# Kernel tuning notes

Hardware: AMD Instinct MI355X
Metric: run time of the kernel (lower is better)

## Reference

```python
import jax, jax.numpy as jnp
import numpy as np

EPS = 1e-5

def _bn(h, gamma, beta):
    # BatchNorm1d in training mode: batch stats over dim 0, biased variance
    mu = h.mean(axis=0)
    var = ((h - mu) ** 2).mean(axis=0)
    return gamma * (h - mu) * jax.lax.rsqrt(var + EPS) + beta

def _gnn_layer(x, w, src, dst, Wv, bv, We, be, g_n, b_n, g_e, b_e):
    n_nodes = x.shape[0]
    # 4 node linears: Wv [4,d,d], bv [4,d]
    xl = jnp.einsum('nd,kfd->knf', x, Wv) + bv[:, None, :]  # [4, N, d]
    x1, x2, x3, x4 = xl[0], xl[1], xl[2], xl[3]
    # sigmoid-gated messages, mean-aggregated to source nodes
    msg = jax.nn.sigmoid(w) * x2[dst]                         # [E, d]
    agg = jax.ops.segment_sum(msg, src, num_segments=n_nodes)
    cnt = jax.ops.segment_sum(jnp.ones((src.shape[0], 1), x.dtype), src,
                              num_segments=n_nodes)
    agg = agg / jnp.maximum(cnt, 1.0)
    x_new = x + jax.nn.silu(_bn(x1 + agg, g_n, b_n))
    w_new = w + jax.nn.silu(_bn(w @ We.T + be + x3[src] + x4[dst], g_e, b_e))
    return x_new, w_new

def setup_inputs() -> dict:
    key = jax.random.key(0)
    N, E, D, L = 50000, 800000, 64, 3
    ks = jax.random.split(key, 10)
    x = jax.random.normal(ks[0], (N, D), dtype=jnp.float32)
    edge_index = jax.random.randint(ks[1], (2, E), 0, N, dtype=jnp.int64)
    edge_attr = jax.random.normal(ks[2], (E, D), dtype=jnp.float32)
    Wv = jax.random.normal(ks[3], (L, 4, D, D), dtype=jnp.float32) * 0.05
    bv = jax.random.normal(ks[4], (L, 4, D), dtype=jnp.float32) * 0.05
    We = jax.random.normal(ks[5], (L, D, D), dtype=jnp.float32) * 0.05
    be = jax.random.normal(ks[6], (L, D), dtype=jnp.float32) * 0.05
    g_node = jnp.ones((L, D), dtype=jnp.float32)
    b_node = jnp.zeros((L, D), dtype=jnp.float32)
    g_edge = jnp.ones((L, D), dtype=jnp.float32)
    b_edge = jnp.zeros((L, D), dtype=jnp.float32)
    return {"x": x, "edge_index": edge_index, "edge_attr": edge_attr,
            "Wv": Wv, "bv": bv, "We": We, "be": be,
            "g_node": g_node, "b_node": b_node,
            "g_edge": g_edge, "b_edge": b_edge}

def reference(x, edge_index, edge_attr, Wv, bv, We, be,
              g_node, b_node, g_edge, b_edge):
    src, dst = edge_index[0], edge_index[1]
    h = jax.nn.silu(x)
    w = jax.nn.silu(edge_attr)
    L = Wv.shape[0]
    for l in range(L):
        h, w = _gnn_layer(h, w, src, dst, Wv[l], bv[l], We[l], be[l],
                          g_node[l], b_node[l], g_edge[l], b_edge[l])
    return h, w
```

## Files before the change

### kernel.cpp

```cpp
#include <hip/hip_runtime.h>

#define NN 50000
#define NE 800000
#define EPSB 1e-5f

typedef __attribute__((ext_vector_type(8))) short bf16x8;
typedef __attribute__((ext_vector_type(8))) unsigned short ushort8;
typedef __attribute__((ext_vector_type(4))) float f32x4;

__device__ __forceinline__ float sigm(float x){ return 1.0f/(1.0f+__expf(-x)); }
__device__ __forceinline__ float silu_(float x){ return x/(1.0f+__expf(-x)); }
__device__ __forceinline__ unsigned int cvt2(float lo, float hi){
  unsigned int r;
  asm("v_cvt_pk_bf16_f32 %0, %1, %2" : "=v"(r) : "v"(lo), "v"(hi));
  return r;
}
__device__ __forceinline__ unsigned short f2bf(float x){
  return (unsigned short)cvt2(x, 0.f);
}
__device__ __forceinline__ float bf2f(unsigned short b){
  return __uint_as_float(((unsigned int)b)<<16);
}
__device__ __forceinline__ ushort8 pack8(float a0,float a1,float a2,float a3,
                                         float a4,float a5,float a6,float a7){
  union { unsigned int u[4]; ushort8 s; } z;
  z.u[0]=cvt2(a0,a1); z.u[1]=cvt2(a2,a3); z.u[2]=cvt2(a4,a5); z.u[3]=cvt2(a6,a7);
  return z.s;
}


__global__ __launch_bounds__(256) void k_deg(const int* __restrict__ src,
                                             int* __restrict__ deg){
  int e = blockIdx.x*256 + threadIdx.x;
  if (e < NE) atomicAdd(&deg[src[e]], 1);
}

__global__ __launch_bounds__(1024) void k_scan(const int* __restrict__ deg,
    int* __restrict__ cursor, float* __restrict__ invd){
  __shared__ int wsum[16];
  __shared__ int sbase;
  if (threadIdx.x == 0) sbase = 0;
  __syncthreads();
  const int lane = threadIdx.x & 63, wid = threadIdx.x >> 6;
  for (int start = 0; start < NN; start += 1024){
    int n = start + (int)threadIdx.x;
    int v = (n < NN) ? deg[n] : 0;
    int x = v;
    #pragma unroll
    for (int d=1; d<64; d<<=1){
      int y = __shfl_up(x, d);
      if (lane >= d) x += y;
    }
    if (lane == 63) wsum[wid] = x;
    __syncthreads();
    if (threadIdx.x < 16){
      int s = wsum[threadIdx.x];
      #pragma unroll
      for (int d=1; d<16; d<<=1){
        int y = __shfl_up(s, d);
        if ((int)threadIdx.x >= d) s += y;
      }
      wsum[threadIdx.x] = s;
    }
    __syncthreads();
    int excl = sbase + ((wid>0)? wsum[wid-1] : 0) + (x - v);
    if (n < NN){
      cursor[n] = excl;
      invd[n] = 1.0f / fmaxf((float)v, 1.0f);
    }
    __syncthreads();
    if (threadIdx.x == 0) sbase += wsum[15];
    __syncthreads();
  }
}

__global__ __launch_bounds__(256) void k_scatter(const int* __restrict__ src,
    const int* __restrict__ dst, int* __restrict__ cursor,
    int* __restrict__ perm, int* __restrict__ ssrc, int* __restrict__ sdst){
  int e = blockIdx.x*256 + threadIdx.x;
  if (e < NE){
    int s = src[e];
    int pos = atomicAdd(&cursor[s], 1);
    perm[pos] = e;
    ssrc[pos] = s;
    sdst[pos] = dst[e];
  }
}

__global__ __launch_bounds__(256) void k_prepW(const float* __restrict__ Wv,
    const float* __restrict__ We,
    unsigned short* __restrict__ wvs, unsigned short* __restrict__ wes){
  const int m = blockIdx.x;
  const float* S = (m < 12) ? (Wv + m*4096) : (We + (m-12)*4096);
  unsigned short* O = (m < 12) ? (wvs + m*4096) : (wes + (m-12)*4096);
  int t = threadIdx.x;
  #pragma unroll
  for (int p=0; p<2; ++p){
    int c = t + p*256;
    int row = c>>3, cc = c&7;
    const float4* sp = (const float4*)(S + row*64 + cc*8);
    float4 a = sp[0], b = sp[1];
    ushort8 v = pack8(a.x,a.y,a.z,a.w,b.x,b.y,b.z,b.w);
    *(ushort8*)((char*)O + ((row*128 + cc*16) ^ ((row&7)<<4))) = v;
  }
}

template<int MODE>
__global__ __launch_bounds__(256) void k_nodelin(const float* __restrict__ xin,
    float* __restrict__ h, float* __restrict__ x1, const float* __restrict__ agg,
    const float* __restrict__ invd, const float* __restrict__ coefp,
    const unsigned short* __restrict__ wvs, const float* __restrict__ bvl,
    unsigned short* __restrict__ xb){
  __shared__ unsigned short shb[4096];
  __shared__ unsigned short sW[4096];
  const int n0 = blockIdx.x*64;
  const int t = threadIdx.x;
  #pragma unroll
  for (int p=0; p<2; ++p){
    int c = t + p*256;
    int row = c>>3, cc = c&7;
    int n = n0 + row;
    ushort8 v = {0,0,0,0,0,0,0,0};
    if (n < NN){
      unsigned base = (unsigned)n*64u + (unsigned)cc*8u;
      float4 a, b;
      if (MODE == 0){
        const float4* xp = (const float4*)(xin + base);
        a = xp[0]; b = xp[1];
        a.x=silu_(a.x); a.y=silu_(a.y); a.z=silu_(a.z); a.w=silu_(a.w);
        b.x=silu_(b.x); b.y=silu_(b.y); b.z=silu_(b.z); b.w=silu_(b.w);
        float4* hp = (float4*)(h + base);
        hp[0] = a; hp[1] = b;
      } else {
        float4* hp = (float4*)(h + base);
        a = hp[0]; b = hp[1];
        const float4* xp = (const float4*)(x1 + base);
        const float4* gp = (const float4*)(agg + base);
        float iv = invd[n];
        float4 xa = xp[0], xb4 = xp[1], ga = gp[0], gb = gp[1];
        float4 s0 = *(const float4*)(coefp + cc*8);
        float4 s1v = *(const float4*)(coefp + cc*8 + 4);
        float4 h0 = *(const float4*)(coefp + 64 + cc*8);
        float4 h1 = *(const float4*)(coefp + 64 + cc*8 + 4);
        a.x += silu_((xa.x + ga.x*iv)*s0.x + h0.x);
        a.y += silu_((xa.y + ga.y*iv)*s0.y + h0.y);
        a.z += silu_((xa.z + ga.z*iv)*s0.z + h0.z);
        a.w += silu_((xa.w + ga.w*iv)*s0.w + h0.w);
        b.x += silu_((xb4.x + gb.x*iv)*s1v.x + h1.x);
        b.y += silu_((xb4.y + gb.y*iv)*s1v.y + h1.y);
        b.z += silu_((xb4.z + gb.z*iv)*s1v.z + h1.z);
        b.w += silu_((xb4.w + gb.w*iv)*s1v.w + h1.w);
        hp[0] = a; hp[1] = b;
      }
      v = pack8(a.x,a.y,a.z,a.w,b.x,b.y,b.z,b.w);
    }
    *(ushort8*)((char*)shb + ((row*128 + cc*16) ^ ((row&7)<<4))) = v;
  }
  __syncthreads();
  const int wid = t>>6, lane = t&63, g = lane>>4, ln = lane&15;
  const int arow = wid*16 + ln;
  bf16x8 afr0 = *(bf16x8*)((char*)shb + ((arow*128 +  0 + g*16) ^ ((arow&7)<<4)));
  bf16x8 afr1 = *(bf16x8*)((char*)shb + ((arow*128 + 64 + g*16) ^ ((arow&7)<<4)));
  for (int k=0; k<4; ++k){
    __syncthreads();
    ((ushort8*)sW)[t]     = ((const ushort8*)(wvs + k*4096))[t];
    ((ushort8*)sW)[t+256] = ((const ushort8*)(wvs + k*4096))[t+256];
    __syncthreads();
    #pragma unroll
    for (int ft=0; ft<4; ++ft){
      int brow = ft*16 + ln;
      bf16x8 b0 = *(bf16x8*)((char*)sW + ((brow*128 +  0 + g*16) ^ ((brow&7)<<4)));
      bf16x8 b1 = *(bf16x8*)((char*)sW + ((brow*128 + 64 + g*16) ^ ((brow&7)<<4)));
      f32x4 c = {0.f,0.f,0.f,0.f};
      c = __builtin_amdgcn_mfma_f32_16x16x32_bf16(afr0, b0, c, 0,0,0);
      c = __builtin_amdgcn_mfma_f32_16x16x32_bf16(afr1, b1, c, 0,0,0);
      float bias = bvl[k*64 + brow];
      #pragma unroll
      for (int r=0; r<4; ++r){
        int n = n0 + wid*16 + g*4 + r;
        if (n < NN){
          float val = c[r] + bias;
          unsigned off = (unsigned)n*64u + (unsigned)brow;
          if (k == 0) x1[off] = val;
          else xb[(unsigned)(k-1)*(NN*64u) + off] = f2bf(val);
        }
      }
    }
  }
}

template<int FIRST>
__global__ __launch_bounds__(256) void k_edgeA(const float* __restrict__ ea,
    unsigned short* __restrict__ wb16,
    const int* __restrict__ perm, const int* __restrict__ ssrc,
    const int* __restrict__ sdst,
    const unsigned short* __restrict__ wes, const float* __restrict__ be,
    const unsigned short* __restrict__ x2, const unsigned short* __restrict__ x3,
    const unsigned short* __restrict__ x4, const float* __restrict__ coefp,
    float* __restrict__ agg, float* __restrict__ esum, float* __restrict__ esq,
    unsigned short* __restrict__ u_bf){
  __shared__ unsigned short sWb[4096];
  __shared__ unsigned short swb[4096];
  __shared__ unsigned short sxs[4096];
  __shared__ int sidx[128];
  const int e0 = blockIdx.x*64;
  const unsigned ebase = (unsigned)e0*64u;
  const int t = threadIdx.x;

  if (t < 64) sidx[t] = ssrc[e0+t];
  else if (t < 128) sidx[t] = sdst[e0+t-64];
  ((ushort8*)sWb)[t]     = ((const ushort8*)wes)[t];
  ((ushort8*)sWb)[t+256] = ((const ushort8*)wes)[t+256];

  #pragma unroll
  for (int p=0; p<2; ++p){
    int c = t + p*256;
    int row = c>>3, cc = c&7;
    ushort8 v;
    if (FIRST){
      unsigned esrc = (unsigned)perm[e0 + row];
      const float4* sp = (const float4*)(ea + esrc*64u + (unsigned)cc*8u);
      float4 a = sp[0], b = sp[1];
      v = pack8(silu_(a.x),silu_(a.y),silu_(a.z),silu_(a.w),
                silu_(b.x),silu_(b.y),silu_(b.z),silu_(b.w));
    } else {
      ushort8 wv = ((const ushort8*)(wb16 + ebase))[c];
      ushort8 uv = ((const ushort8*)(u_bf + ebase))[c];
      int f0 = cc*8;
      float4 s0 = *(const float4*)(coefp + 128 + f0);
      float4 s1v = *(const float4*)(coefp + 128 + f0 + 4);
      float4 h0 = *(const float4*)(coefp + 192 + f0);
      float4 h1 = *(const float4*)(coefp + 192 + f0 + 4);
      v = pack8(
        bf2f(wv[0]) + silu_(bf2f(uv[0])*s0.x + h0.x),
        bf2f(wv[1]) + silu_(bf2f(uv[1])*s0.y + h0.y),
        bf2f(wv[2]) + silu_(bf2f(uv[2])*s0.z + h0.z),
        bf2f(wv[3]) + silu_(bf2f(uv[3])*s0.w + h0.w),
        bf2f(wv[4]) + silu_(bf2f(uv[4])*s1v.x + h1.x),
        bf2f(wv[5]) + silu_(bf2f(uv[5])*s1v.y + h1.y),
        bf2f(wv[6]) + silu_(bf2f(uv[6])*s1v.z + h1.z),
        bf2f(wv[7]) + silu_(bf2f(uv[7])*s1v.w + h1.w));
    }
    ((ushort8*)(wb16 + ebase))[c] = v;
    *(ushort8*)((char*)swb + ((row*128 + cc*16) ^ ((row&7)<<4))) = v;
  }
  __syncthreads();

  #pragma unroll
  for (int p=0; p<2; ++p){
    int c = t + p*256;
    int row = c>>3, cc = c&7;
    unsigned s  = (unsigned)sidx[row];
    unsigned d2 = (unsigned)sidx[64+row];
    ushort8 a = *(const ushort8*)(x3 + s*64u  + (unsigned)cc*8u);
    ushort8 b = *(const ushort8*)(x4 + d2*64u + (unsigned)cc*8u);
    ushort8 v = pack8(
      bf2f(a[0])+bf2f(b[0]), bf2f(a[1])+bf2f(b[1]),
      bf2f(a[2])+bf2f(b[2]), bf2f(a[3])+bf2f(b[3]),
      bf2f(a[4])+bf2f(b[4]), bf2f(a[5])+bf2f(b[5]),
      bf2f(a[6])+bf2f(b[6]), bf2f(a[7])+bf2f(b[7]));
    *(ushort8*)((char*)sxs + ((row*128 + cc*16) ^ ((row&7)<<4))) = v;
  }

  const int wid = t>>6, lane = t&63, g = lane>>4, ln = lane&15;
  const int arow = wid*16 + ln;
  bf16x8 afr0 = *(bf16x8*)((char*)swb + ((arow*128 +  0 + g*16) ^ ((arow&7)<<4)));
  bf16x8 afr1 = *(bf16x8*)((char*)swb + ((arow*128 + 64 + g*16) ^ ((arow&7)<<4)));
  bf16x8 bfr[4][2];
  #pragma unroll
  for (int ft=0; ft<4; ++ft){
    int brow = ft*16 + ln;
    bfr[ft][0] = *(bf16x8*)((char*)sWb + ((brow*128 +  0 + g*16) ^ ((brow&7)<<4)));
    bfr[ft][1] = *(bf16x8*)((char*)sWb + ((brow*128 + 64 + g*16) ^ ((brow&7)<<4)));
  }
  __syncthreads();

  f32x4 cacc[4];
  #pragma unroll
  for (int ft=0; ft<4; ++ft){
    f32x4 c = {0.f,0.f,0.f,0.f};
    c = __builtin_amdgcn_mfma_f32_16x16x32_bf16(afr0, bfr[ft][0], c, 0,0,0);
    c = __builtin_amdgcn_mfma_f32_16x16x32_bf16(afr1, bfr[ft][1], c, 0,0,0);
    cacc[ft] = c;
  }

  float bef[4];
  #pragma unroll
  for (int ft=0; ft<4; ++ft) bef[ft] = be[ft*16+ln];
  float s1[4]={0.f,0.f,0.f,0.f}, s2[4]={0.f,0.f,0.f,0.f};
  #pragma unroll
  for (int r=0; r<4; ++r){
    int row = wid*16 + g*4 + r;
    #pragma unroll
    for (int ft=0; ft<4; ++ft){
      int f = ft*16 + ln;
      unsigned short a34 = *(unsigned short*)((char*)sxs + ((row*128 + f*2) ^ ((row&7)<<4)));
      float u = cacc[ft][r] + bef[ft] + bf2f(a34);
      s1[ft] += u; s2[ft] += u*u;
      *(unsigned short*)((char*)sWb + ((row*128 + f*2) ^ ((row&7)<<4))) = f2bf(u);
    }
  }
  #pragma unroll
  for (int ft=0; ft<4; ++ft){
    s1[ft] += __shfl_xor(s1[ft], 16); s1[ft] += __shfl_xor(s1[ft], 32);
    s2[ft] += __shfl_xor(s2[ft], 16); s2[ft] += __shfl_xor(s2[ft], 32);
  }
  if (g == 0){
    int slot = ((blockIdx.x<<2) + wid) & 63;
    #pragma unroll
    for (int ft=0; ft<4; ++ft){
      atomicAdd(&esum[(slot<<6) + ft*16 + ln], s1[ft]);
      atomicAdd(&esq [(slot<<6) + ft*16 + ln], s2[ft]);
    }
  }
  __syncthreads();

  #pragma unroll
  for (int p=0; p<2; ++p){
    int c = t + p*256;
    int row = c>>3, cc = c&7;
    ushort8 v = *(ushort8*)((char*)sWb + ((row*128 + cc*16) ^ ((row&7)<<4)));
    ((ushort8*)(u_bf + ebase))[c] = v;
    unsigned d2 = (unsigned)sidx[64+row];
    ushort8 xv = *(const ushort8*)(x2 + d2*64u + (unsigned)cc*8u);
    *(ushort8*)((char*)sxs + ((row*128 + cc*16) ^ ((row&7)<<4))) = xv;
  }
  __syncthreads();

  {
    const int el0 = wid<<4;
    unsigned curs = (unsigned)sidx[el0];
    float run = 0.f;
    #pragma unroll
    for (int j=0; j<16; ++j){
      int el = el0 + j;
      unsigned s = (unsigned)sidx[el];
      if (s != curs){
        atomicAdd(&agg[curs*64u + (unsigned)lane], run);
        run = 0.f; curs = s;
      }
      unsigned short wv = *(unsigned short*)((char*)swb + ((el*128 + lane*2) ^ ((el&7)<<4)));
      unsigned short xv = *(unsigned short*)((char*)sxs + ((el*128 + lane*2) ^ ((el&7)<<4)));
      run += sigm(bf2f(wv)) * bf2f(xv);
    }
    atomicAdd(&agg[curs*64u + (unsigned)lane], run);
  }
}

__global__ __launch_bounds__(256) void k_nodestats(const float* __restrict__ x1,
    const float* __restrict__ agg, const float* __restrict__ invd,
    float* __restrict__ nsum, float* __restrict__ nsq){
  const int f = threadIdx.x & 63, sub = threadIdx.x >> 6;
  float s1=0.f, s2=0.f;
  for (int n = blockIdx.x*4 + sub; n < NN; n += gridDim.x*4){
    unsigned off = (unsigned)n*64u + (unsigned)f;
    float t = x1[off] + agg[off]*invd[n];
    s1 += t; s2 += t*t;
  }
  __shared__ float red[4][64][2];
  red[sub][f][0]=s1; red[sub][f][1]=s2;
  __syncthreads();
  if (sub==0){
    float a1=red[0][f][0]+red[1][f][0]+red[2][f][0]+red[3][f][0];
    float a2=red[0][f][1]+red[1][f][1]+red[2][f][1]+red[3][f][1];
    int slot = blockIdx.x & 63;
    atomicAdd(&nsum[(slot<<6)+f], a1);
    atomicAdd(&nsq[(slot<<6)+f], a2);
  }
}

__global__ void k_finalize(const float* __restrict__ nsum, const float* __restrict__ nsq,
    const float* __restrict__ esum, const float* __restrict__ esq,
    const float* __restrict__ gn, const float* __restrict__ bn,
    const float* __restrict__ ge, const float* __restrict__ beb,
    float* __restrict__ coef){
  int t = threadIdx.x;
  if (t >= 128) return;
  int f = t & 63;
  const float* S1 = (t<64)? nsum : esum;
  const float* S2 = (t<64)? nsq  : esq;
  float cnt = (t<64)? (float)NN : (float)NE;
  float s1=0.f, s2=0.f;
  for (int k=0;k<64;++k){ s1 += S1[(k<<6)+f]; s2 += S2[(k<<6)+f]; }
  float mu = s1/cnt;
  float var = s2/cnt - mu*mu;
  float rstd = rsqrtf(var + EPSB);
  float g = (t<64)? gn[f] : ge[f];
  float b = (t<64)? bn[f] : beb[f];
  float sc = g*rstd, sh = b - mu*sc;
  coef[((t<64)?0:2)*64 + f] = sc;
  coef[((t<64)?1:3)*64 + f] = sh;
}

__global__ __launch_bounds__(256) void k_nodeupd(const float* __restrict__ x1,
    const float* __restrict__ agg, const float* __restrict__ invd,
    const float* __restrict__ coef, float* __restrict__ h){
  unsigned i = blockIdx.x*256u + threadIdx.x;
  if (i >= NN*64u) return;
  unsigned n = i>>6, f = i&63u;
  float t = x1[i] + agg[i]*invd[n];
  float v = t*coef[f] + coef[64+f];
  h[i] += silu_(v);
}

__global__ __launch_bounds__(256) void k_edgeBfin(const unsigned short* __restrict__ wb16,
    const unsigned short* __restrict__ u_bf, const float* __restrict__ coef,
    const int* __restrict__ perm, float* __restrict__ wout){
  unsigned i = blockIdx.x*256u + threadIdx.x;
  unsigned cc = i & 7u, f0 = cc*8u;
  unsigned eid = (unsigned)perm[i>>3];
  ushort8 wv = ((const ushort8*)wb16)[i];
  ushort8 ub = ((const ushort8*)u_bf)[i];
  float4 s0 = *(const float4*)(coef + 128 + f0);
  float4 s1v = *(const float4*)(coef + 128 + f0 + 4);
  float4 h0 = *(const float4*)(coef + 192 + f0);
  float4 h1 = *(const float4*)(coef + 192 + f0 + 4);
  float4 oa, ob;
  oa.x = bf2f(wv[0]) + silu_(bf2f(ub[0])*s0.x + h0.x);
  oa.y = bf2f(wv[1]) + silu_(bf2f(ub[1])*s0.y + h0.y);
  oa.z = bf2f(wv[2]) + silu_(bf2f(ub[2])*s0.z + h0.z);
  oa.w = bf2f(wv[3]) + silu_(bf2f(ub[3])*s0.w + h0.w);
  ob.x = bf2f(wv[4]) + silu_(bf2f(ub[4])*s1v.x + h1.x);
  ob.y = bf2f(wv[5]) + silu_(bf2f(ub[5])*s1v.y + h1.y);
  ob.z = bf2f(wv[6]) + silu_(bf2f(ub[6])*s1v.z + h1.z);
  ob.w = bf2f(wv[7]) + silu_(bf2f(ub[7])*s1v.w + h1.w);
  float4* wp = (float4*)(wout + eid*64u + f0);
  wp[0] = oa; wp[1] = ob;
}


extern "C" void kernel_launch(void* const* d_in, const int* in_sizes, int n_in,
                              void* d_out, int out_size, void* d_ws, size_t ws_size,
                              hipStream_t stream){
  const float* x      = (const float*)d_in[0];
  const int*   eidx   = (const int*)d_in[1];
  const float* eattr  = (const float*)d_in[2];
  const float* Wv     = (const float*)d_in[3];
  const float* bv     = (const float*)d_in[4];
  const float* We     = (const float*)d_in[5];
  const float* be     = (const float*)d_in[6];
  const float* g_node = (const float*)d_in[7];
  const float* b_node = (const float*)d_in[8];
  const float* g_edge = (const float*)d_in[9];
  const float* b_edge = (const float*)d_in[10];
  const int* src = eidx;
  const int* dst = eidx + NE;

  float* hout = (float*)d_out;
  float* wout = hout + (size_t)NN*64;

  float* W    = (float*)d_ws;
  float* x1   = W;
  float* agg  = W + 3200000;
  float* nsum = W + 6400000;
  float* nsq  = W + 6404096;
  float* esum = W + 6408192;
  float* esq  = W + 6412288;
  float* coef = W + 6416384;
  float* invd = W + 6417152;
  int*   deg  = (int*)(W + 6467152);
  unsigned short* xb   = (unsigned short*)(W + 6517152);
  unsigned short* wvs  = (unsigned short*)(W + 11317152);
  unsigned short* wes  = (unsigned short*)(W + 11341728);
  unsigned short* u_bf = (unsigned short*)(W + 11347872);
  unsigned short* wb16 = (unsigned short*)(W + 36947872);
  int* perm   = (int*)(W + 62547872);
  int* ssrc   = (int*)(W + 63347872);
  int* sdst   = (int*)(W + 64147872);
  int* cursor = (int*)(W + 64947872);

  hipMemsetAsync(deg, 0, NN*sizeof(int), stream);
  k_deg<<<3125, 256, 0, stream>>>(src, deg);
  k_scan<<<1, 1024, 0, stream>>>(deg, cursor, invd);
  k_scatter<<<3125, 256, 0, stream>>>(src, dst, cursor, perm, ssrc, sdst);
  k_prepW<<<15, 256, 0, stream>>>(Wv, We, wvs, wes);

  const unsigned short* x2 = xb;
  const unsigned short* x3 = xb + (size_t)NN*64;
  const unsigned short* x4 = xb + (size_t)2*NN*64;

  for (int l=0; l<3; ++l){
    const float* cprev = coef + (l-1)*256;
    if (l == 0)
      k_nodelin<0><<<782, 256, 0, stream>>>(x, hout, x1, agg, invd, coef,
          wvs + l*16384, bv + l*256, xb);
    else
      k_nodelin<1><<<782, 256, 0, stream>>>(x, hout, x1, agg, invd, cprev,
          wvs + l*16384, bv + l*256, xb);
    hipMemsetAsync(agg, 0, (3200000 + 4*4096)*sizeof(float), stream);
    if (l == 0)
      k_edgeA<1><<<12500, 256, 0, stream>>>(eattr, wb16, perm, ssrc, sdst,
          wes + l*4096, be + l*64, x2, x3, x4, coef, agg, esum, esq, u_bf);
    else
      k_edgeA<0><<<12500, 256, 0, stream>>>(eattr, wb16, perm, ssrc, sdst,
          wes + l*4096, be + l*64, x2, x3, x4, cprev, agg, esum, esq, u_bf);
    k_nodestats<<<128, 256, 0, stream>>>(x1, agg, invd, nsum, nsq);
    k_finalize<<<1, 128, 0, stream>>>(nsum, nsq, esum, esq,
        g_node + l*64, b_node + l*64, g_edge + l*64, b_edge + l*64, coef + l*256);
  }
  k_nodeupd<<<12500, 256, 0, stream>>>(x1, agg, invd, coef + 512, hout);
  k_edgeBfin<<<25000, 256, 0, stream>>>(wb16, u_bf, coef + 512, perm, wout);
}
```

Before: 796.6 us.

## Recompute edge pre-activation instead of storing u_bf; double-buffer node projections

The bf16 edge pre-activation buffer is no longer stored. Each edge kernel instead recomputes the previous layer's edge linear with MFMA, using the old weights and double-buffered x3/x4 node projections, so it can apply the previous update before the current layer. This removes a 100 MB-per-layer write and read of u_bf at the cost of a second GEMM and extra gathers. The agg and stats buffers are also zeroed inside the consuming kernels rather than by per-layer memsets, and the final edge pass is replaced with a recompute kernel.

```diff
diff --git a/kernel.cpp b/kernel.cpp
--- a/kernel.cpp
+++ b/kernel.cpp
@@ -26,6 +26,12 @@
   union { unsigned int u[4]; ushort8 s; } z;
   z.u[0]=cvt2(a0,a1); z.u[1]=cvt2(a2,a3); z.u[2]=cvt2(a4,a5); z.u[3]=cvt2(a6,a7);
   return z.s;
+}
+__device__ __forceinline__ ushort8 sum8(ushort8 a, ushort8 b){
+  return pack8(bf2f(a[0])+bf2f(b[0]), bf2f(a[1])+bf2f(b[1]),
+               bf2f(a[2])+bf2f(b[2]), bf2f(a[3])+bf2f(b[3]),
+               bf2f(a[4])+bf2f(b[4]), bf2f(a[5])+bf2f(b[5]),
+               bf2f(a[6])+bf2f(b[6]), bf2f(a[7])+bf2f(b[7]));
 }
 
 
@@ -107,7 +113,7 @@
 
 template<int MODE>
 __global__ __launch_bounds__(256) void k_nodelin(const float* __restrict__ xin,
-    float* __restrict__ h, float* __restrict__ x1, const float* __restrict__ agg,
+    float* __restrict__ h, float* __restrict__ x1, float* __restrict__ agg,
     const float* __restrict__ invd, const float* __restrict__ coefp,
     const unsigned short* __restrict__ wvs, const float* __restrict__ bvl,
     unsigned short* __restrict__ xb){
@@ -135,9 +141,11 @@
         float4* hp = (float4*)(h + base);
         a = hp[0]; b = hp[1];
         const float4* xp = (const float4*)(x1 + base);
-        const float4* gp = (const float4*)(agg + base);
+        float4* gp = (float4*)(agg + base);
         float iv = invd[n];
         float4 xa = xp[0], xb4 = xp[1], ga = gp[0], gb = gp[1];
+        float4 z = make_float4(0.f,0.f,0.f,0.f);
+        gp[0] = z; gp[1] = z;
         float4 s0 = *(const float4*)(coefp + cc*8);
         float4 s1v = *(const float4*)(coefp + cc*8 + 4);
         float4 h0 = *(const float4*)(coefp + 64 + cc*8);
@@ -194,11 +202,12 @@
     unsigned short* __restrict__ wb16,
     const int* __restrict__ perm, const int* __restrict__ ssrc,
     const int* __restrict__ sdst,
-    const unsigned short* __restrict__ wes, const float* __restrict__ be,
-    const unsigned short* __restrict__ x2, const unsigned short* __restrict__ x3,
-    const unsigned short* __restrict__ x4, const float* __restrict__ coefp,
-    float* __restrict__ agg, float* __restrict__ esum, float* __restrict__ esq,
-    unsigned short* __restrict__ u_bf){
+    const unsigned short* __restrict__ wesO, const unsigned short* __restrict__ wesN,
+    const float* __restrict__ beO, const float* __restrict__ beN,
+    const unsigned short* __restrict__ x3o, const unsigned short* __restrict__ x4o,
+    const unsigned short* __restrict__ x2n, const unsigned short* __restrict__ x3n,
+    const unsigned short* __restrict__ x4n, const float* __restrict__ coefp,
+    float* __restrict__ agg, float* __restrict__ esum, float* __restrict__ esq){
   __shared__ unsigned short sWb[4096];
   __shared__ unsigned short swb[4096];
   __shared__ unsigned short sxs[4096];
@@ -206,64 +215,119 @@
   const int e0 = blockIdx.x*64;
   const unsigned ebase = (unsigned)e0*64u;
   const int t = threadIdx.x;
+  const int row0 = t>>3, cc8 = t&7, rr1 = row0+32;
+  const int wid = t>>6, lane = t&63, g = lane>>4, ln = lane&15;
+  const int arow = wid*16 + ln;
+
+  unsigned sA0=(unsigned)ssrc[e0+row0], dA0=(unsigned)sdst[e0+row0];
+  unsigned sA1=(unsigned)ssrc[e0+rr1],  dA1=(unsigned)sdst[e0+rr1];
 
   if (t < 64) sidx[t] = ssrc[e0+t];
   else if (t < 128) sidx[t] = sdst[e0+t-64];
-  ((ushort8*)sWb)[t]     = ((const ushort8*)wes)[t];
-  ((ushort8*)sWb)[t+256] = ((const ushort8*)wes)[t+256];
-
+
+  {
+    const unsigned short* wesP = FIRST ? wesN : wesO;
+    ((ushort8*)sWb)[t]     = ((const ushort8*)wesP)[t];
+    ((ushort8*)sWb)[t+256] = ((const ushort8*)wesP)[t+256];
+  }
   #pragma unroll
   for (int p=0; p<2; ++p){
     int c = t + p*256;
-    int row = c>>3, cc = c&7;
+    int row = row0 + p*32;
     ushort8 v;
     if (FIRST){
       unsigned esrc = (unsigned)perm[e0 + row];
-      const float4* sp = (const float4*)(ea + esrc*64u + (unsigned)cc*8u);
+      const float4* sp = (const float4*)(ea + esrc*64u + (unsigned)cc8*8u);
       float4 a = sp[0], b = sp[1];
       v = pack8(silu_(a.x),silu_(a.y),silu_(a.z),silu_(a.w),
                 silu_(b.x),silu_(b.y),silu_(b.z),silu_(b.w));
+      ((ushort8*)(wb16 + ebase))[c] = v;
     } else {
-      ushort8 wv = ((const ushort8*)(wb16 + ebase))[c];
-      ushort8 uv = ((const ushort8*)(u_bf + ebase))[c];
-      int f0 = cc*8;
-      float4 s0 = *(const float4*)(coefp + 128 + f0);
-      float4 s1v = *(const float4*)(coefp + 128 + f0 + 4);
-      float4 h0 = *(const float4*)(coefp + 192 + f0);
-      float4 h1 = *(const float4*)(coefp + 192 + f0 + 4);
-      v = pack8(
-        bf2f(wv[0]) + silu_(bf2f(uv[0])*s0.x + h0.x),
-        bf2f(wv[1]) + silu_(bf2f(uv[1])*s0.y + h0.y),
-        bf2f(wv[2]) + silu_(bf2f(uv[2])*s0.z + h0.z),
-        bf2f(wv[3]) + silu_(bf2f(uv[3])*s0.w + h0.w),
-        bf2f(wv[4]) + silu_(bf2f(uv[4])*s1v.x + h1.x),
-        bf2f(wv[5]) + silu_(bf2f(uv[5])*s1v.y + h1.y),
-        bf2f(wv[6]) + silu_(bf2f(uv[6])*s1v.z + h1.z),
-        bf2f(wv[7]) + silu_(bf2f(uv[7])*s1v.w + h1.w));
-    }
-    ((ushort8*)(wb16 + ebase))[c] = v;
-    *(ushort8*)((char*)swb + ((row*128 + cc*16) ^ ((row&7)<<4))) = v;
-  }
-  __syncthreads();
-
-  #pragma unroll
-  for (int p=0; p<2; ++p){
-    int c = t + p*256;
-    int row = c>>3, cc = c&7;
-    unsigned s  = (unsigned)sidx[row];
-    unsigned d2 = (unsigned)sidx[64+row];
-    ushort8 a = *(const ushort8*)(x3 + s*64u  + (unsigned)cc*8u);
-    ushort8 b = *(const ushort8*)(x4 + d2*64u + (unsigned)cc*8u);
-    ushort8 v = pack8(
-      bf2f(a[0])+bf2f(b[0]), bf2f(a[1])+bf2f(b[1]),
-      bf2f(a[2])+bf2f(b[2]), bf2f(a[3])+bf2f(b[3]),
-      bf2f(a[4])+bf2f(b[4]), bf2f(a[5])+bf2f(b[5]),
-      bf2f(a[6])+bf2f(b[6]), bf2f(a[7])+bf2f(b[7]));
-    *(ushort8*)((char*)sxs + ((row*128 + cc*16) ^ ((row&7)<<4))) = v;
-  }
-
-  const int wid = t>>6, lane = t&63, g = lane>>4, ln = lane&15;
-  const int arow = wid*16 + ln;
+      v = ((const ushort8*)(wb16 + ebase))[c];
+    }
+    *(ushort8*)((char*)swb + ((row*128 + cc8*16) ^ ((row&7)<<4))) = v;
+  }
+  {
+    const unsigned short* X3 = FIRST ? x3n : x3o;
+    const unsigned short* X4 = FIRST ? x4n : x4o;
+    ushort8 a0 = *(const ushort8*)(X3 + sA0*64u + (unsigned)cc8*8u);
+    ushort8 b0 = *(const ushort8*)(X4 + dA0*64u + (unsigned)cc8*8u);
+    ushort8 a1 = *(const ushort8*)(X3 + sA1*64u + (unsigned)cc8*8u);
+    ushort8 b1 = *(const ushort8*)(X4 + dA1*64u + (unsigned)cc8*8u);
+    *(ushort8*)((char*)sxs + ((row0*128 + cc8*16) ^ ((row0&7)<<4))) = sum8(a0,b0);
+    *(ushort8*)((char*)sxs + ((rr1*128  + cc8*16) ^ ((rr1&7)<<4)))  = sum8(a1,b1);
+  }
+  __syncthreads();
+
+  if (!FIRST){
+    bf16x8 afr0 = *(bf16x8*)((char*)swb + ((arow*128 +  0 + g*16) ^ ((arow&7)<<4)));
+    bf16x8 afr1 = *(bf16x8*)((char*)swb + ((arow*128 + 64 + g*16) ^ ((arow&7)<<4)));
+    bf16x8 bfr[4][2];
+    #pragma unroll
+    for (int ft=0; ft<4; ++ft){
+      int brow = ft*16 + ln;
+      bfr[ft][0] = *(bf16x8*)((char*)sWb + ((brow*128 +  0 + g*16) ^ ((brow&7)<<4)));
+      bfr[ft][1] = *(bf16x8*)((char*)sWb + ((brow*128 + 64 + g*16) ^ ((brow&7)<<4)));
+    }
+    f32x4 cacc[4];
+    #pragma unroll
+    for (int ft=0; ft<4; ++ft){
+      f32x4 c = {0.f,0.f,0.f,0.f};
+      c = __builtin_amdgcn_mfma_f32_16x16x32_bf16(afr0, bfr[ft][0], c, 0,0,0);
+      c = __builtin_amdgcn_mfma_f32_16x16x32_bf16(afr1, bfr[ft][1], c, 0,0,0);
+      cacc[ft] = c;
+    }
+    float scp[4], shp[4], beo[4], wnew[4][4];
+    #pragma unroll
+    for (int ft=0; ft<4; ++ft){
+      scp[ft] = coefp[128 + ft*16 + ln];
+      shp[ft] = coefp[192 + ft*16 + ln];
+      beo[ft] = beO[ft*16 + ln];
+    }
+    #pragma unroll
+    for (int r=0; r<4; ++r){
+      int row = wid*16 + g*4 + r;
+      #pragma unroll
+      for (int ft=0; ft<4; ++ft){
+        int f = ft*16 + ln;
+        unsigned short a34 = *(unsigned short*)((char*)sxs + ((row*128 + f*2) ^ ((row&7)<<4)));
+        unsigned short wo  = *(unsigned short*)((char*)swb + ((row*128 + f*2) ^ ((row&7)<<4)));
+        float u = cacc[ft][r] + beo[ft] + bf2f(a34);
+        wnew[ft][r] = bf2f(wo) + silu_(u*scp[ft] + shp[ft]);
+      }
+    }
+    __syncthreads();
+
+    #pragma unroll
+    for (int r=0; r<4; ++r){
+      int row = wid*16 + g*4 + r;
+      #pragma unroll
+      for (int ft=0; ft<4; ++ft){
+        int f = ft*16 + ln;
+        *(unsigned short*)((char*)swb + ((row*128 + f*2) ^ ((row&7)<<4))) = f2bf(wnew[ft][r]);
+      }
+    }
+    ((ushort8*)sWb)[t]     = ((const ushort8*)wesN)[t];
+    ((ushort8*)sWb)[t+256] = ((const ushort8*)wesN)[t+256];
+    {
+      ushort8 a0 = *(const ushort8*)(x3n + sA0*64u + (unsigned)cc8*8u);
+      ushort8 b0 = *(const ushort8*)(x4n + dA0*64u + (unsigned)cc8*8u);
+      ushort8 a1 = *(const ushort8*)(x3n + sA1*64u + (unsigned)cc8*8u);
+      ushort8 b1 = *(const ushort8*)(x4n + dA1*64u + (unsigned)cc8*8u);
+      *(ushort8*)((char*)sxs + ((row0*128 + cc8*16) ^ ((row0&7)<<4))) = sum8(a0,b0);
+      *(ushort8*)((char*)sxs + ((rr1*128  + cc8*16) ^ ((rr1&7)<<4)))  = sum8(a1,b1);
+    }
+    __syncthreads();
+
+    #pragma unroll
+    for (int p=0; p<2; ++p){
+      int c = t + p*256;
+      int row = row0 + p*32;
+      ushort8 v = *(ushort8*)((char*)swb + ((row*128 + cc8*16) ^ ((row&7)<<4)));
+      ((ushort8*)(wb16 + ebase))[c] = v;
+    }
+  }
+
   bf16x8 afr0 = *(bf16x8*)((char*)swb + ((arow*128 +  0 + g*16) ^ ((arow&7)<<4)));
   bf16x8 afr1 = *(bf16x8*)((char*)swb + ((arow*128 + 64 + g*16) ^ ((arow&7)<<4)));
   bf16x8 bfr[4][2];
@@ -273,8 +337,6 @@
     bfr[ft][0] = *(bf16x8*)((char*)sWb + ((brow*128 +  0 + g*16) ^ ((brow&7)<<4)));
     bfr[ft][1] = *(bf16x8*)((char*)sWb + ((brow*128 + 64 + g*16) ^ ((brow&7)<<4)));
   }
-  __syncthreads();
-
   f32x4 cacc[4];
   #pragma unroll
   for (int ft=0; ft<4; ++ft){
@@ -283,11 +345,9 @@
     c = __builtin_amdgcn_mfma_f32_16x16x32_bf16(afr1, bfr[ft][1], c, 0,0,0);
     cacc[ft] = c;
   }
-
-  float bef[4];
-  #pragma unroll
-  for (int ft=0; ft<4; ++ft) bef[ft] = be[ft*16+ln];
-  float s1[4]={0.f,0.f,0.f,0.f}, s2[4]={0.f,0.f,0.f,0.f};
+  float ben[4], s1[4]={0.f,0.f,0.f,0.f}, s2[4]={0.f,0.f,0.f,0.f};
+  #pragma unroll
+  for (int ft=0; ft<4; ++ft) ben[ft] = beN[ft*16+ln];
   #pragma unroll
   for (int r=0; r<4; ++r){
     int row = wid*16 + g*4 + r;
@@ -295,9 +355,8 @@
     for (int ft=0; ft<4; ++ft){
       int f = ft*16 + ln;
       unsigned short a34 = *(unsigned short*)((char*)sxs + ((row*128 + f*2) ^ ((row&7)<<4)));
-      float u = cacc[ft][r] + bef[ft] + bf2f(a34);
+      float u = cacc[ft][r] + ben[ft] + bf2f(a34);
       s1[ft] += u; s2[ft] += u*u;
-      *(unsigned short*)((char*)sWb + ((row*128 + f*2) ^ ((row&7)<<4))) = f2bf(u);
     }
   }
   #pragma unroll
@@ -315,15 +374,11 @@
   }
   __syncthreads();
 
-  #pragma unroll
-  for (int p=0; p<2; ++p){
-    int c = t + p*256;
-    int row = c>>3, cc = c&7;
-    ushort8 v = *(ushort8*)((char*)sWb + ((row*128 + cc*16) ^ ((row&7)<<4)));
-    ((ushort8*)(u_bf + ebase))[c] = v;
-    unsigned d2 = (unsigned)sidx[64+row];
-    ushort8 xv = *(const ushort8*)(x2 + d2*64u + (unsigned)cc*8u);
-    *(ushort8*)((char*)sxs + ((row*128 + cc*16) ^ ((row&7)<<4))) = xv;
+  {
+    ushort8 v0 = *(const ushort8*)(x2n + dA0*64u + (unsigned)cc8*8u);
+    ushort8 v1 = *(const ushort8*)(x2n + dA1*64u + (unsigned)cc8*8u);
+    *(ushort8*)((char*)sxs + ((row0*128 + cc8*16) ^ ((row0&7)<<4))) = v0;
+    *(ushort8*)((char*)sxs + ((rr1*128  + cc8*16) ^ ((rr1&7)<<4)))  = v1;
   }
   __syncthreads();
 
@@ -347,6 +402,96 @@
   }
 }
 
+__global__ __launch_bounds__(256) void k_edgeFin(const unsigned short* __restrict__ wb16,
+    const int* __restrict__ perm, const int* __restrict__ ssrc,
+    const int* __restrict__ sdst,
+    const unsigned short* __restrict__ wes2, const float* __restrict__ be2,
+    const unsigned short* __restrict__ x3c, const unsigned short* __restrict__ x4c,
+    const float* __restrict__ coef2, float* __restrict__ wout){
+  __shared__ unsigned short sWb[4096];
+  __shared__ unsigned short swb[4096];
+  __shared__ unsigned short sxs[4096];
+  const int e0 = blockIdx.x*64;
+  const unsigned ebase = (unsigned)e0*64u;
+  const int t = threadIdx.x;
+  const int row0 = t>>3, cc8 = t&7, rr1 = row0+32;
+  const int wid = t>>6, lane = t&63, g = lane>>4, ln = lane&15;
+  const int arow = wid*16 + ln;
+
+  unsigned sA0=(unsigned)ssrc[e0+row0], dA0=(unsigned)sdst[e0+row0];
+  unsigned sA1=(unsigned)ssrc[e0+rr1],  dA1=(unsigned)sdst[e0+rr1];
+
+  ((ushort8*)sWb)[t]     = ((const ushort8*)wes2)[t];
+  ((ushort8*)sWb)[t+256] = ((const ushort8*)wes2)[t+256];
+  #pragma unroll
+  for (int p=0; p<2; ++p){
+    int c = t + p*256;
+    int row = row0 + p*32;
+    ushort8 v = ((const ushort8*)(wb16 + ebase))[c];
+    *(ushort8*)((char*)swb + ((row*128 + cc8*16) ^ ((row&7)<<4))) = v;
+  }
+  {
+    ushort8 a0 = *(const ushort8*)(x3c + sA0*64u + (unsigned)cc8*8u);
+    ushort8 b0 = *(const ushort8*)(x4c + dA0*64u + (unsigned)cc8*8u);
+    ushort8 a1 = *(const ushort8*)(x3c + sA1*64u + (unsigned)cc8*8u);
+    ushort8 b1 = *(const ushort8*)(x4c + dA1*64u + (unsigned)cc8*8u);
+    *(ushort8*)((char*)sxs + ((row0*128 + cc8*16) ^ ((row0&7)<<4))) = sum8(a0,b0);
+    *(ushort8*)((char*)sxs + ((rr1*128  + cc8*16) ^ ((rr1&7)<<4)))  = sum8(a1,b1);
+  }
+  __syncthreads();
+
+  bf16x8 afr0 = *(bf16x8*)((char*)swb + ((arow*128 +  0 + g*16) ^ ((arow&7)<<4)));
+  bf16x8 afr1 = *(bf16x8*)((char*)swb + ((arow*128 + 64 + g*16) ^ ((arow&7)<<4)));
+  bf16x8 bfr[4][2];
+  #pragma unroll
+  for (int ft=0; ft<4; ++ft){
+    int brow = ft*16 + ln;
+    bfr[ft][0] = *(bf16x8*)((char*)sWb + ((brow*128 +  0 + g*16) ^ ((brow&7)<<4)));
+    bfr[ft][1] = *(bf16x8*)((char*)sWb + ((brow*128 + 64 + g*16) ^ ((brow&7)<<4)));
+  }
+  f32x4 cacc[4];
+  #pragma unroll
+  for (int ft=0; ft<4; ++ft){
+    f32x4 c = {0.f,0.f,0.f,0.f};
+    c = __builtin_amdgcn_mfma_f32_16x16x32_bf16(afr0, bfr[ft][0], c, 0,0,0);
+    c = __builtin_amdgcn_mfma_f32_16x16x32_bf16(afr1, bfr[ft][1], c, 0,0,0);
+    cacc[ft] = c;
+  }
+  float scp[4], shp[4], be4[4];
+  #pragma unroll
+  for (int ft=0; ft<4; ++ft){
+    scp[ft] = coef2[128 + ft*16 + ln];
+    shp[ft] = coef2[192 + ft*16 + ln];
+    be4[ft] = be2[ft*16 + ln];
+  }
+  #pragma unroll
+  for (int r=0; r<4; ++r){
+    int row = wid*16 + g*4 + r;
+    #pragma unroll
+    for (int ft=0; ft<4; ++ft){
+      int f = ft*16 + ln;
+      unsigned short* slot = (unsigned short*)((char*)sxs + ((row*128 + f*2) ^ ((row&7)<<4)));
+      unsigned short wo = *(unsigned short*)((char*)swb + ((row*128 + f*2) ^ ((row&7)<<4)));
+      float u = cacc[ft][r] + be4[ft] + bf2f(*slot);
+      float o = bf2f(wo) + silu_(u*scp[ft] + shp[ft]);
+      *slot = f2bf(o);
+    }
+  }
+  __syncthreads();
+
+  #pragma unroll
+  for (int p=0; p<2; ++p){
+    int c = t + p*256;
+    int row = row0 + p*32;
+    ushort8 v = *(ushort8*)((char*)sxs + ((row*128 + cc8*16) ^ ((row&7)<<4)));
+    unsigned eid = (unsigned)perm[e0 + row];
+    float4 oa = make_float4(bf2f(v[0]),bf2f(v[1]),bf2f(v[2]),bf2f(v[3]));
+    float4 ob = make_float4(bf2f(v[4]),bf2f(v[5]),bf2f(v[6]),bf2f(v[7]));
+    float4* wp = (float4*)(wout + eid*64u + (unsigned)cc8*8u);
+    wp[0] = oa; wp[1] = ob;
+  }
+}
+
 __global__ __launch_bounds__(256) void k_nodestats(const float* __restrict__ x1,
     const float* __restrict__ agg, const float* __restrict__ invd,
     float* __restrict__ nsum, float* __restrict__ nsq){
@@ -369,19 +514,20 @@
   }
 }
 
-__global__ void k_finalize(const float* __restrict__ nsum, const float* __restrict__ nsq,
-    const float* __restrict__ esum, const float* __restrict__ esq,
+__global__ void k_finalize(float* __restrict__ nsum, float* __restrict__ nsq,
+    float* __restrict__ esum, float* __restrict__ esq,
     const float* __restrict__ gn, const float* __restrict__ bn,
     const float* __restrict__ ge, const float* __restrict__ beb,
     float* __restrict__ coef){
   int t = threadIdx.x;
   if (t >= 128) return;
   int f = t & 63;
-  const float* S1 = (t<64)? nsum : esum;
-  const float* S2 = (t<64)? nsq  : esq;
+  float* S1 = (t<64)? nsum : esum;
+  float* S2 = (t<64)? nsq  : esq;
   float cnt = (t<64)? (float)NN : (float)NE;
   float s1=0.f, s2=0.f;
   for (int k=0;k<64;++k){ s1 += S1[(k<<6)+f]; s2 += S2[(k<<6)+f]; }
+  for (int k=0;k<64;++k){ S1[(k<<6)+f]=0.f; S2[(k<<6)+f]=0.f; }
   float mu = s1/cnt;
   float var = s2/cnt - mu*mu;
   float rstd = rsqrtf(var + EPSB);
@@ -401,31 +547,6 @@
   float t = x1[i] + agg[i]*invd[n];
   float v = t*coef[f] + coef[64+f];
   h[i] += silu_(v);
-}
-
-__global__ __launch_bounds__(256) void k_edgeBfin(const unsigned short* __restrict__ wb16,
-    const unsigned short* __restrict__ u_bf, const float* __restrict__ coef,
-    const int* __restrict__ perm, float* __restrict__ wout){
-  unsigned i = blockIdx.x*256u + threadIdx.x;
-  unsigned cc = i & 7u, f0 = cc*8u;
-  unsigned eid = (unsigned)perm[i>>3];
-  ushort8 wv = ((const ushort8*)wb16)[i];
-  ushort8 ub = ((const ushort8*)u_bf)[i];
-  float4 s0 = *(const float4*)(coef + 128 + f0);
-  float4 s1v = *(const float4*)(coef + 128 + f0 + 4);
-  float4 h0 = *(const float4*)(coef + 192 + f0);
-  float4 h1 = *(const float4*)(coef + 192 + f0 + 4);
-  float4 oa, ob;
-  oa.x = bf2f(wv[0]) + silu_(bf2f(ub[0])*s0.x + h0.x);
-  oa.y = bf2f(wv[1]) + silu_(bf2f(ub[1])*s0.y + h0.y);
-  oa.z = bf2f(wv[2]) + silu_(bf2f(ub[2])*s0.z + h0.z);
-  oa.w = bf2f(wv[3]) + silu_(bf2f(ub[3])*s0.w + h0.w);
-  ob.x = bf2f(wv[4]) + silu_(bf2f(ub[4])*s1v.x + h1.x);
-  ob.y = bf2f(wv[5]) + silu_(bf2f(ub[5])*s1v.y + h1.y);
-  ob.z = bf2f(wv[6]) + silu_(bf2f(ub[6])*s1v.z + h1.z);
-  ob.w = bf2f(wv[7]) + silu_(bf2f(ub[7])*s1v.w + h1.w);
-  float4* wp = (float4*)(wout + eid*64u + f0);
-  wp[0] = oa; wp[1] = ob;
 }
 
 
@@ -460,44 +581,51 @@
   float* invd = W + 6417152;
   int*   deg  = (int*)(W + 6467152);
   unsigned short* xb   = (unsigned short*)(W + 6517152);
-  unsigned short* wvs  = (unsigned short*)(W + 11317152);
-  unsigned short* wes  = (unsigned short*)(W + 11341728);
-  unsigned short* u_bf = (unsigned short*)(W + 11347872);
-  unsigned short* wb16 = (unsigned short*)(W + 36947872);
-  int* perm   = (int*)(W + 62547872);
-  int* ssrc   = (int*)(W + 63347872);
-  int* sdst   = (int*)(W + 64147872);
-  int* cursor = (int*)(W + 64947872);
+  unsigned short* wvs  = (unsigned short*)(W + 16200000);
+  unsigned short* wes  = (unsigned short*)(W + 16230000);
+  unsigned short* wb16 = (unsigned short*)(W + 16240000);
+  int* perm   = (int*)(W + 41840000);
+  int* ssrc   = (int*)(W + 42640000);
+  int* sdst   = (int*)(W + 43440000);
+  int* cursor = (int*)(W + 44240000);
 
   hipMemsetAsync(deg, 0, NN*sizeof(int), stream);
+  hipMemsetAsync(agg, 0, (3200000 + 4*4096)*sizeof(float), stream);
   k_deg<<<3125, 256, 0, stream>>>(src, deg);
   k_scan<<<1, 1024, 0, stream>>>(deg, cursor, invd);
   k_scatter<<<3125, 256, 0, stream>>>(src, dst, cursor, perm, ssrc, sdst);
   k_prepW<<<15, 256, 0, stream>>>(Wv, We, wvs, wes);
 
-  const unsigned short* x2 = xb;
-  const unsigned short* x3 = xb + (size_t)NN*64;
-  const unsigned short* x4 = xb + (size_t)2*NN*64;
-
+  const unsigned N64 = NN*64u;
   for (int l=0; l<3; ++l){
+    int gc = l & 1, go = (l-1) & 1;
+    unsigned short* xbc = xb + (size_t)gc*3*N64;
+    unsigned short* xbo = xb + (size_t)go*3*N64;
     const float* cprev = coef + (l-1)*256;
     if (l == 0)
       k_nodelin<0><<<782, 256, 0, stream>>>(x, hout, x1, agg, invd, coef,
-          wvs + l*16384, bv + l*256, xb);
+          wvs + l*16384, bv + l*256, xbc);
     else
       k_nodelin<1><<<782, 256, 0, stream>>>(x, hout, x1, agg, invd, cprev,
-          wvs + l*16384, bv + l*256, xb);
-    hipMemsetAsync(agg, 0, (3200000 + 4*4096)*sizeof(float), stream);
+          wvs + l*16384, bv + l*256, xbc);
     if (l == 0)
       k_edgeA<1><<<12500, 256, 0, stream>>>(eattr, wb16, perm, ssrc, sdst,
-          wes + l*4096, be + l*64, x2, x3, x4, coef, agg, esum, esq, u_bf);
+          wes, wes, be, be,
+          xbo + N64, xbo + 2*N64,
+          xbc, xbc + N64, xbc + 2*N64,
+          coef, agg, esum, esq);
     else
       k_edgeA<0><<<12500, 256, 0, stream>>>(eattr, wb16, perm, ssrc, sdst,
-          wes + l*4096, be + l*64, x2, x3, x4, cprev, agg, esum, esq, u_bf);
+          wes + (l-1)*4096, wes + l*4096, be + (l-1)*64, be + l*64,
+          xbo + N64, xbo + 2*N64,
+          xbc, xbc + N64, xbc + 2*N64,
+          cprev, agg, esum, esq);
     k_nodestats<<<128, 256, 0, stream>>>(x1, agg, invd, nsum, nsq);
     k_finalize<<<1, 128, 0, stream>>>(nsum, nsq, esum, esq,
         g_node + l*64, b_node + l*64, g_edge + l*64, b_edge + l*64, coef + l*256);
   }
+  unsigned short* xb2 = xb;
   k_nodeupd<<<12500, 256, 0, stream>>>(x1, agg, invd, coef + 512, hout);
-  k_edgeBfin<<<25000, 256, 0, stream>>>(wb16, u_bf, coef + 512, perm, wout);
-}
+  k_edgeFin<<<12500, 256, 0, stream>>>(wb16, perm, ssrc, sdst,
+      wes + 2*4096, be + 2*64, xb2 + N64, xb2 + 2*N64, coef + 512, wout);
+}
```

Result: faster. 768.9 us (-3.5%).
